# Kernel optimization log

Hardware: AMD Instinct MI355X
Metric: run time of the kernel (lower is better)

Reference implementation:

```python
import jax, jax.numpy as jnp
import numpy as np

N = 65536
E = 1048576
IN_DIM, HID, OUT = 500, 256, 64
ALPHA = 0.1
K = 10


def setup_inputs() -> dict:
    key = jax.random.key(0)
    ks = jax.random.split(key, 12)
    x = jax.random.normal(ks[0], (N, IN_DIM), dtype=jnp.float32)
    edge_row = jax.random.randint(ks[1], (E,), 0, N, dtype=jnp.int32)
    edge_col = jax.random.randint(ks[2], (E,), 0, N, dtype=jnp.int32)
    edge_weight = jax.random.uniform(ks[3], (E,), dtype=jnp.float32)
    # Linear params (Kaiming-uniform-like scale)
    def lin(k, fan_in, fan_out):
        kw, kb = jax.random.split(k)
        bound = 1.0 / np.sqrt(fan_in)
        W = jax.random.uniform(kw, (fan_in, fan_out), minval=-bound, maxval=bound, dtype=jnp.float32)
        b = jax.random.uniform(kb, (fan_out,), minval=-bound, maxval=bound, dtype=jnp.float32)
        return W, b
    W1, b1 = lin(ks[4], IN_DIM, HID)
    W2, b2 = lin(ks[5], HID, HID)
    W3, b3 = lin(ks[6], HID, OUT)
    return {"x": x, "W1": W1, "b1": b1, "W2": W2, "b2": b2,
            "W3": W3, "b3": b3, "edge_weight": edge_weight,
            "edge_row": edge_row, "edge_col": edge_col}


def reference(x, W1, b1, W2, b2, W3, b3, edge_weight, edge_row, edge_col):
    # MLP stack (dropout=0.0, norm_type='none')
    h = jax.nn.relu(x @ W1 + b1)          # [N, HID]
    h = jax.nn.relu(h @ W2 + b2)          # [N, HID]
    h = h @ W3 + b3                        # [N, OUT]
    h0 = h
    w = edge_weight[:, None]               # [E, 1]
    # APPNP: k steps of h = (1-alpha) * (A @ h) + alpha * h0 (SpMM via segment_sum)
    def step(h, _):
        msg = h[edge_col] * w               # [E, OUT] gather + scale
        agg = jax.ops.segment_sum(msg, edge_row, num_segments=N)  # [N, OUT]
        return (1.0 - ALPHA) * agg + ALPHA * h0, None
    h, _ = jax.lax.scan(step, h, None, length=K)
    return h
```

## Files before the change

kernel.cpp:

```cpp
#include <hip/hip_runtime.h>
#include <cstdint>
#include <cstddef>


#define N_NODES   65536
#define N_EDGES   1048576
#define IN_DIM    500
#define IN_PAD    512
#define HID_DIM   256
#define OUT_DIM   64
#define K_STEPS   10

#define NPW   8
#define CAPW  608
#define NCHUNK 16

typedef _Float16 half8 __attribute__((ext_vector_type(8)));
typedef __fp16   fp16x2 __attribute__((ext_vector_type(2)));
typedef float    f32x4 __attribute__((ext_vector_type(4)));

#define HA_OFF    0ULL
#define HB_OFF    33554432ULL
#define H1_OFF    67108864ULL
#define H0_OFF    67108864ULL
#define H2_OFF    100663296ULL
#define CNT2_OFF  100663296ULL
#define RANK_OFF  104857600ULL
#define TOT_OFF   109051904ULL
#define W1T_OFF   134217728ULL
#define W2T_OFF   134479872ULL
#define W3T_OFF   134610944ULL
#define ROWP_OFF  134643712ULL
#define EDG_OFF   135430400ULL

__device__ __forceinline__ void gload_lds16(const void* g, void* l) {
  __builtin_amdgcn_global_load_lds(
      (const __attribute__((address_space(1))) void*)g,
      (__attribute__((address_space(3))) void*)l, 16, 0, 0);
}

__device__ __forceinline__ unsigned short f2bf_rne(float f) {
  unsigned u = __float_as_uint(f);
  u += 0x7fffu + ((u >> 16) & 1u);
  return (unsigned short)(u >> 16);
}
__device__ __forceinline__ float uaf(unsigned u) {
  return __uint_as_float(u);
}
__device__ __forceinline__ float lo16(unsigned v) {
  return __uint_as_float(v << 16);
}
__device__ __forceinline__ float hi16(unsigned v) {
  return __uint_as_float(v & 0xffff0000u);
}

template <int TM, int TN, int WM, int WN, bool RELU, int OMODE>
__global__ __launch_bounds__(256)
void gemm_kernel(const _Float16* __restrict__ A, const _Float16* __restrict__ B,
                 const float* __restrict__ bias, void* __restrict__ Cout,
                 int M, int Nn, int K) {
  static_assert((TM * 8) % 256 == 0 && (TN * 8) % 256 == 0, "tile");
  __shared__ uint4 As[TM * 8];
  __shared__ uint4 Bs[TN * 8];
  const int t    = threadIdx.x;
  const int lane = t & 63;
  const int wave = t >> 6;
  const int wm   = wave / WN;
  const int wn   = wave % WN;
  const int row0 = blockIdx.x * TM;
  const int col0 = blockIdx.y * TN;
  const int l15  = lane & 15;
  const int lq   = lane >> 4;

  f32x4 acc[4][4];
#pragma unroll
  for (int i = 0; i < 4; ++i)
#pragma unroll
    for (int j = 0; j < 4; ++j) acc[i][j] = (f32x4){0.f, 0.f, 0.f, 0.f};

  for (int k0 = 0; k0 < K; k0 += 64) {
#pragma unroll
    for (int i = 0; i < (TM * 8) / 256; ++i) {
      const int c = i * 256 + wave * 64 + lane;
      const int q = c / TM;
      const int r = c % TM;
      gload_lds16(A + (size_t)(row0 + r) * K + (k0 + q * 8),
                  As + i * 256 + wave * 64);
    }
#pragma unroll
    for (int i = 0; i < (TN * 8) / 256; ++i) {
      const int c = i * 256 + wave * 64 + lane;
      const int q = c / TN;
      const int r = c % TN;
      gload_lds16(B + (size_t)(col0 + r) * K + (k0 + q * 8),
                  Bs + i * 256 + wave * 64);
    }
    __syncthreads();
#pragma unroll
    for (int kk = 0; kk < 2; ++kk) {
      const int qa = kk * 4 + lq;
      half8 af[4], bfr[4];
#pragma unroll
      for (int mt = 0; mt < 4; ++mt)
        af[mt] = *((const half8*)(As + (qa * TM + wm * 64 + mt * 16 + l15)));
#pragma unroll
      for (int nt = 0; nt < 4; ++nt)
        bfr[nt] = *((const half8*)(Bs + (qa * TN + wn * 64 + nt * 16 + l15)));
#pragma unroll
      for (int mt = 0; mt < 4; ++mt)
#pragma unroll
        for (int nt = 0; nt < 4; ++nt)
          acc[mt][nt] = __builtin_amdgcn_mfma_f32_16x16x32_f16(
              af[mt], bfr[nt], acc[mt][nt], 0, 0, 0);
    }
    __syncthreads();
  }

#pragma unroll
  for (int mt = 0; mt < 4; ++mt) {
#pragma unroll
    for (int nt = 0; nt < 4; ++nt) {
      const int col = col0 + wn * 64 + nt * 16 + l15;
      const float bv = bias[col];
#pragma unroll
      for (int r = 0; r < 4; ++r) {
        const int row = row0 + wm * 64 + mt * 16 + lq * 4 + r;
        float v = acc[mt][nt][r] + bv;
        if (RELU) v = fmaxf(v, 0.f);
        if (OMODE == 0)
          ((_Float16*)Cout)[(size_t)row * Nn + col] = (_Float16)v;
        else if (OMODE == 1)
          ((unsigned short*)Cout)[(size_t)row * Nn + col] = f2bf_rne(v);
        else
          ((float*)Cout)[(size_t)row * Nn + col] = v;
      }
    }
  }
}

__global__ __launch_bounds__(256)
void gemm1_f32(const float* __restrict__ x, const _Float16* __restrict__ B,
               const float* __restrict__ bias, _Float16* __restrict__ C) {
  __shared__ uint4 As[16 * 128];
  __shared__ uint4 Bs[8 * 256];
  const int t    = threadIdx.x;
  const int lane = t & 63;
  const int wave = t >> 6;
  const int row0 = blockIdx.x * 128;
  const int l15  = lane & 15;
  const int lq   = lane >> 4;

  f32x4 acc[8][4];
#pragma unroll
  for (int i = 0; i < 8; ++i)
#pragma unroll
    for (int j = 0; j < 4; ++j) acc[i][j] = (f32x4){0.f, 0.f, 0.f, 0.f};

  for (int k0 = 0; k0 < IN_PAD; k0 += 64) {
#pragma unroll
    for (int i = 0; i < 8; ++i) {
      const int c = i * 256 + t;
      const int q = c >> 7;
      const int r = c & 127;
      int kb = k0 + q * 4;
      if (kb >= IN_DIM) kb = 0;
      gload_lds16(x + (size_t)(row0 + r) * IN_DIM + kb, As + q * 128 + r);
    }
#pragma unroll
    for (int i = 0; i < 8; ++i) {
      const int c = i * 256 + t;
      const int q = c >> 8;
      const int r = c & 255;
      gload_lds16(B + (size_t)r * IN_PAD + (k0 + q * 8), Bs + q * 256 + r);
    }
    __syncthreads();
#pragma unroll
    for (int kk = 0; kk < 2; ++kk) {
      const int qa = kk * 4 + lq;
      half8 bfr[4];
#pragma unroll
      for (int nt = 0; nt < 4; ++nt)
        bfr[nt] = *((const half8*)(Bs + qa * 256 + wave * 64 + nt * 16 + l15));
#pragma unroll
      for (int mt = 0; mt < 8; ++mt) {
        const uint4 lo = As[(qa * 2 + 0) * 128 + mt * 16 + l15];
        const uint4 hi = As[(qa * 2 + 1) * 128 + mt * 16 + l15];
        half8 af;
        fp16x2 p;
        p = __builtin_amdgcn_cvt_pkrtz(uaf(lo.x), uaf(lo.y));
        af[0] = p[0]; af[1] = p[1];
        p = __builtin_amdgcn_cvt_pkrtz(uaf(lo.z), uaf(lo.w));
        af[2] = p[0]; af[3] = p[1];
        p = __builtin_amdgcn_cvt_pkrtz(uaf(hi.x), uaf(hi.y));
        af[4] = p[0]; af[5] = p[1];
        p = __builtin_amdgcn_cvt_pkrtz(uaf(hi.z), uaf(hi.w));
        af[6] = p[0]; af[7] = p[1];
#pragma unroll
        for (int nt = 0; nt < 4; ++nt)
          acc[mt][nt] = __builtin_amdgcn_mfma_f32_16x16x32_f16(
              af, bfr[nt], acc[mt][nt], 0, 0, 0);
      }
    }
    __syncthreads();
  }

#pragma unroll
  for (int mt = 0; mt < 8; ++mt) {
#pragma unroll
    for (int nt = 0; nt < 4; ++nt) {
      const int col = wave * 64 + nt * 16 + l15;
      const float bv = bias[col];
#pragma unroll
      for (int r = 0; r < 4; ++r) {
        const int row = row0 + mt * 16 + lq * 4 + r;
        const float v = fmaxf(acc[mt][nt][r] + bv, 0.f);
        C[(size_t)row * HID_DIM + col] = (_Float16)v;
      }
    }
  }
}

__global__ void cast_w_kernel(const float* __restrict__ W,
                              _Float16* __restrict__ Wt, int K, int Kpad,
                              int Nn) {
  const int idx = blockIdx.x * blockDim.x + threadIdx.x;
  if (idx >= Nn * Kpad) return;
  const int n = idx / Kpad;
  const int k = idx % Kpad;
  const float v = (k < K) ? W[(size_t)k * Nn + n] : 0.f;
  Wt[idx] = (_Float16)v;
}

__global__ void hist2_kernel(const int* __restrict__ row,
                             int* __restrict__ cnt2, int* __restrict__ rank,
                             int E) {
  const int e = blockIdx.x * blockDim.x + threadIdx.x;
  if (e < E)
    rank[e] = atomicAdd(&cnt2[(e >> 16) * N_NODES + row[e]], 1);
}

__global__ void scan_tot_kernel(const int* __restrict__ cnt2,
                                int* __restrict__ tot) {
  const int r = blockIdx.x * blockDim.x + threadIdx.x;
  int s = 0;
#pragma unroll
  for (int c = 0; c < NCHUNK; ++c) s += cnt2[c * N_NODES + r];
  tot[r] = s;
}

__global__ void scan_kernel(const int4* __restrict__ counts4,
                            int* __restrict__ rowptr) {
  __shared__ int part[1024];
  const int t = threadIdx.x;
  const int base = t * 16;
  int4 c[16];
  int s = 0;
#pragma unroll
  for (int i = 0; i < 16; ++i) {
    c[i] = counts4[base + i];
    s += c[i].x + c[i].y + c[i].z + c[i].w;
  }
  part[t] = s;
  __syncthreads();
  for (int off = 1; off < 1024; off <<= 1) {
    const int v = (t >= off) ? part[t - off] : 0;
    __syncthreads();
    part[t] += v;
    __syncthreads();
  }
  int run = (t == 0) ? 0 : part[t - 1];
#pragma unroll
  for (int i = 0; i < 16; ++i) {
    int4 r;
    r.x = run; run += c[i].x;
    r.y = run; run += c[i].y;
    r.z = run; run += c[i].z;
    r.w = run; run += c[i].w;
    ((int4*)rowptr)[base + i] = r;
  }
  if (t == 1023) rowptr[N_NODES] = run;
}

__global__ void chunkbase_kernel(int* __restrict__ cnt2,
                                 const int* __restrict__ rowptr) {
  const int r = blockIdx.x * blockDim.x + threadIdx.x;
  int run = rowptr[r];
#pragma unroll
  for (int c = 0; c < NCHUNK; ++c) {
    const int t = cnt2[c * N_NODES + r];
    cnt2[c * N_NODES + r] = run;
    run += t;
  }
}

__global__ void scatter2_kernel(const int* __restrict__ row,
                                const int* __restrict__ col,
                                const float* __restrict__ w,
                                const int* __restrict__ rank,
                                const int* __restrict__ cbase,
                                int2* __restrict__ edges, int E) {
  const int e = blockIdx.x * blockDim.x + threadIdx.x;
  if (e < E) {
    const int pos = cbase[(e >> 16) * N_NODES + row[e]] + rank[e];
    edges[pos] = make_int2(col[e], __float_as_int(w[e]));
  }
}

template <bool OUT_F32>
__global__ __launch_bounds__(256)
void prop_step(const unsigned short* __restrict__ hin,
               const unsigned short* __restrict__ h0,
               void* __restrict__ hout, const int* __restrict__ rowptr,
               const int2* __restrict__ edges) {
  __shared__ int2 eb[4][CAPW];
  const int wave = threadIdx.x >> 6;
  const int lane = threadIdx.x & 63;
  const int half = lane >> 5;
  const int lp   = lane & 31;
  const int node0 = (blockIdx.x * 4 + wave) * NPW;
  const unsigned* __restrict__ hin32 = (const unsigned*)hin;
  const unsigned* __restrict__ h032  = (const unsigned*)h0;

  const int rp  = rowptr[node0 + min(lane, NPW)];
  const int beg = __shfl(rp, 0);
  const int nE  = __shfl(rp, NPW) - beg;
  const int rrel = rp - beg;
  int2* __restrict__ ebw = eb[wave];

  const bool fast = (nE <= CAPW);
  if (fast) {
    for (int i = lane; i < nE; i += 64) ebw[i] = edges[beg + i];
    __builtin_amdgcn_s_waitcnt(0);
  }

  for (int i = 0; i < NPW; ++i) {
    const int nb = __shfl(rrel, i);
    const int ne = __shfl(rrel, i + 1);
    float ax0 = 0.f, ay0 = 0.f, ax1 = 0.f, ay1 = 0.f;
    int j = nb;
    if (fast) {
      for (; j + 8 <= ne; j += 8) {
        const int2 e0 = ebw[j + 0 + half];
        const int2 e1 = ebw[j + 2 + half];
        const int2 e2 = ebw[j + 4 + half];
        const int2 e3 = ebw[j + 6 + half];
        const unsigned v0 = hin32[(e0.x << 5) | lp];
        const unsigned v1 = hin32[(e1.x << 5) | lp];
        const unsigned v2 = hin32[(e2.x << 5) | lp];
        const unsigned v3 = hin32[(e3.x << 5) | lp];
        const float w0 = uaf(e0.y), w1 = uaf(e1.y);
        const float w2 = uaf(e2.y), w3 = uaf(e3.y);
        ax0 = fmaf(w0, lo16(v0), ax0); ay0 = fmaf(w0, hi16(v0), ay0);
        ax1 = fmaf(w1, lo16(v1), ax1); ay1 = fmaf(w1, hi16(v1), ay1);
        ax0 = fmaf(w2, lo16(v2), ax0); ay0 = fmaf(w2, hi16(v2), ay0);
        ax1 = fmaf(w3, lo16(v3), ax1); ay1 = fmaf(w3, hi16(v3), ay1);
      }
      for (; j + 2 <= ne; j += 2) {
        const int2 e = ebw[j + half];
        const unsigned v = hin32[(e.x << 5) | lp];
        const float w = uaf(e.y);
        ax0 = fmaf(w, lo16(v), ax0); ay0 = fmaf(w, hi16(v), ay0);
      }
      if (j < ne) {
        const int2 e = ebw[j];
        const unsigned v = hin32[(e.x << 5) | lp];
        const float w = half ? 0.f : uaf(e.y);
        ax0 = fmaf(w, lo16(v), ax0); ay0 = fmaf(w, hi16(v), ay0);
      }
    } else {
      for (; j < ne; j += 2) {
        const int idx = j + half;
        const int2 e = edges[beg + (idx < ne ? idx : ne - 1)];
        const float w = (idx < ne) ? uaf(e.y) : 0.f;
        const unsigned v = hin32[(e.x << 5) | lp];
        ax0 = fmaf(w, lo16(v), ax0); ay0 = fmaf(w, hi16(v), ay0);
      }
    }
    float sx = ax0 + ax1;
    float sy = ay0 + ay1;
    sx += __shfl_xor(sx, 32);
    sy += __shfl_xor(sy, 32);
    const int o32 = ((node0 + i) << 5) | lp;
    const unsigned h0v = h032[o32];
    const float r0 = 0.9f * sx + 0.1f * lo16(h0v);
    const float r1 = 0.9f * sy + 0.1f * hi16(h0v);
    if (half == 0) {
      if (OUT_F32) {
        ((float2*)hout)[o32] = make_float2(r0, r1);
      } else {
        ((unsigned*)hout)[o32] =
            (unsigned)f2bf_rne(r0) | ((unsigned)f2bf_rne(r1) << 16);
      }
    }
  }
}

extern "C" void kernel_launch(void* const* d_in, const int* in_sizes, int n_in,
                              void* d_out, int out_size, void* d_ws,
                              size_t ws_size, hipStream_t stream) {
  const float* x  = (const float*)d_in[0];
  const float* W1 = (const float*)d_in[1];
  const float* b1 = (const float*)d_in[2];
  const float* W2 = (const float*)d_in[3];
  const float* b2 = (const float*)d_in[4];
  const float* W3 = (const float*)d_in[5];
  const float* b3 = (const float*)d_in[6];
  const float* ew = (const float*)d_in[7];
  const int* erow = (const int*)d_in[8];
  const int* ecol = (const int*)d_in[9];

  char* ws = (char*)d_ws;
  _Float16* h1  = (_Float16*)(ws + H1_OFF);
  _Float16* h2  = (_Float16*)(ws + H2_OFF);
  _Float16* w1t = (_Float16*)(ws + W1T_OFF);
  _Float16* w2t = (_Float16*)(ws + W2T_OFF);
  _Float16* w3t = (_Float16*)(ws + W3T_OFF);
  unsigned short* h0b = (unsigned short*)(ws + H0_OFF);
  unsigned short* hAb = (unsigned short*)(ws + HA_OFF);
  unsigned short* hBb = (unsigned short*)(ws + HB_OFF);
  int* rowp     = (int*)(ws + ROWP_OFF);
  int* cnt2     = (int*)(ws + CNT2_OFF);
  int* rankb    = (int*)(ws + RANK_OFF);
  int* tot      = (int*)(ws + TOT_OFF);
  int2* edges   = (int2*)(ws + EDG_OFF);
  float* outp   = (float*)d_out;

  hipMemsetAsync(cnt2, 0, NCHUNK * N_NODES * sizeof(int), stream);
  hist2_kernel<<<N_EDGES / 256, 256, 0, stream>>>(erow, cnt2, rankb, N_EDGES);
  scan_tot_kernel<<<N_NODES / 256, 256, 0, stream>>>(cnt2, tot);
  scan_kernel<<<1, 1024, 0, stream>>>((const int4*)tot, rowp);
  chunkbase_kernel<<<N_NODES / 256, 256, 0, stream>>>(cnt2, rowp);
  scatter2_kernel<<<N_EDGES / 256, 256, 0, stream>>>(erow, ecol, ew, rankb,
                                                     cnt2, edges, N_EDGES);

  cast_w_kernel<<<(HID_DIM * IN_PAD) / 256, 256, 0, stream>>>(W1, w1t, IN_DIM,
                                                              IN_PAD, HID_DIM);
  cast_w_kernel<<<(HID_DIM * HID_DIM) / 256, 256, 0, stream>>>(
      W2, w2t, HID_DIM, HID_DIM, HID_DIM);
  cast_w_kernel<<<(OUT_DIM * HID_DIM) / 256, 256, 0, stream>>>(
      W3, w3t, HID_DIM, HID_DIM, OUT_DIM);

  gemm1_f32<<<dim3(N_NODES / 128), 256, 0, stream>>>(x, w1t, b1, h1);
  gemm_kernel<128, 128, 2, 2, true, 0>
      <<<dim3(N_NODES / 128, HID_DIM / 128), 256, 0, stream>>>(
          h1, w2t, b2, h2, N_NODES, HID_DIM, HID_DIM);
  gemm_kernel<256, 64, 4, 1, false, 1>
      <<<dim3(N_NODES / 256, 1), 256, 0, stream>>>(h2, w3t, b3, h0b, N_NODES,
                                                   OUT_DIM, HID_DIM);

  for (int s = 0; s < K_STEPS - 1; ++s) {
    const unsigned short* hin = (s == 0) ? h0b : ((s - 1) & 1 ? hBb : hAb);
    unsigned short* hout = (s & 1) ? hBb : hAb;
    prop_step<false><<<N_NODES / (4 * NPW), 256, 0, stream>>>(hin, h0b, hout,
                                                              rowp, edges);
  }
  prop_step<true><<<N_NODES / (4 * NPW), 256, 0, stream>>>(
      (K_STEPS - 2) & 1 ? hBb : hAb, h0b, outp, rowp, edges);
}
```

Measured before the change: 629.2 us.

## Fuse all propagation steps into one cooperative persistent kernel with grid sync

Replaces the ten separate prop_step launches with one cooperative kernel. It loops over the K steps and calls grid.sync between them, ping-ponging the bf16 buffers and writing fp32 output on the last step. Each wave now handles 16 nodes with a larger LDS edge buffer, so its edge slice is loaded into LDS once and reused across all steps instead of being reread from global memory each step. In exchange it pays grid-wide barrier costs and caps residency at 4 blocks per CU. The launch only works if all 1024 blocks can be co-resident, and fewer waves are left to hide gather latency.

Result: slower. 1.822 ms (+189.5%).

```diff
diff --git a/kernel.cpp b/kernel.cpp
--- a/kernel.cpp
+++ b/kernel.cpp
@@ -1,6 +1,9 @@
 #include <hip/hip_runtime.h>
+#include <hip/hip_cooperative_groups.h>
 #include <cstdint>
 #include <cstddef>
+
+namespace cg = cooperative_groups;
 
 
 #define N_NODES   65536
@@ -11,8 +14,8 @@
 #define OUT_DIM   64
 #define K_STEPS   10
 
-#define NPW   8
-#define CAPW  608
+#define NPW   16
+#define CAPW  1152
 #define NCHUNK 16
 
 typedef _Float16 half8 __attribute__((ext_vector_type(8)));
@@ -306,20 +309,18 @@
   }
 }
 
-template <bool OUT_F32>
-__global__ __launch_bounds__(256)
-void prop_step(const unsigned short* __restrict__ hin,
-               const unsigned short* __restrict__ h0,
-               void* __restrict__ hout, const int* __restrict__ rowptr,
+__global__ __launch_bounds__(256, 4)
+void prop_coop(const unsigned* __restrict__ h0g,
+               unsigned* __restrict__ hA, unsigned* __restrict__ hB,
+               float* __restrict__ outp, const int* __restrict__ rowptr,
                const int2* __restrict__ edges) {
   __shared__ int2 eb[4][CAPW];
+  cg::grid_group grid = cg::this_grid();
   const int wave = threadIdx.x >> 6;
   const int lane = threadIdx.x & 63;
   const int half = lane >> 5;
   const int lp   = lane & 31;
   const int node0 = (blockIdx.x * 4 + wave) * NPW;
-  const unsigned* __restrict__ hin32 = (const unsigned*)hin;
-  const unsigned* __restrict__ h032  = (const unsigned*)h0;
 
   const int rp  = rowptr[node0 + min(lane, NPW)];
   const int beg = __shfl(rp, 0);
@@ -333,65 +334,73 @@
     __builtin_amdgcn_s_waitcnt(0);
   }
 
-  for (int i = 0; i < NPW; ++i) {
-    const int nb = __shfl(rrel, i);
-    const int ne = __shfl(rrel, i + 1);
-    float ax0 = 0.f, ay0 = 0.f, ax1 = 0.f, ay1 = 0.f;
-    int j = nb;
-    if (fast) {
-      for (; j + 8 <= ne; j += 8) {
-        const int2 e0 = ebw[j + 0 + half];
-        const int2 e1 = ebw[j + 2 + half];
-        const int2 e2 = ebw[j + 4 + half];
-        const int2 e3 = ebw[j + 6 + half];
-        const unsigned v0 = hin32[(e0.x << 5) | lp];
-        const unsigned v1 = hin32[(e1.x << 5) | lp];
-        const unsigned v2 = hin32[(e2.x << 5) | lp];
-        const unsigned v3 = hin32[(e3.x << 5) | lp];
-        const float w0 = uaf(e0.y), w1 = uaf(e1.y);
-        const float w2 = uaf(e2.y), w3 = uaf(e3.y);
-        ax0 = fmaf(w0, lo16(v0), ax0); ay0 = fmaf(w0, hi16(v0), ay0);
-        ax1 = fmaf(w1, lo16(v1), ax1); ay1 = fmaf(w1, hi16(v1), ay1);
-        ax0 = fmaf(w2, lo16(v2), ax0); ay0 = fmaf(w2, hi16(v2), ay0);
-        ax1 = fmaf(w3, lo16(v3), ax1); ay1 = fmaf(w3, hi16(v3), ay1);
+  for (int s = 0; s < K_STEPS; ++s) {
+    const bool last = (s == K_STEPS - 1);
+    const unsigned* __restrict__ hin32 =
+        (s == 0) ? h0g : (((s - 1) & 1) ? hB : hA);
+    unsigned* __restrict__ houtb = (s & 1) ? hB : hA;
+
+    for (int i = 0; i < NPW; ++i) {
+      const int nb = __shfl(rrel, i);
+      const int ne = __shfl(rrel, i + 1);
+      float ax0 = 0.f, ay0 = 0.f, ax1 = 0.f, ay1 = 0.f;
+      int j = nb;
+      if (fast) {
+        for (; j + 8 <= ne; j += 8) {
+          const int2 e0 = ebw[j + 0 + half];
+          const int2 e1 = ebw[j + 2 + half];
+          const int2 e2 = ebw[j + 4 + half];
+          const int2 e3 = ebw[j + 6 + half];
+          const unsigned v0 = hin32[(e0.x << 5) | lp];
+          const unsigned v1 = hin32[(e1.x << 5) | lp];
+          const unsigned v2 = hin32[(e2.x << 5) | lp];
+          const unsigned v3 = hin32[(e3.x << 5) | lp];
+          const float w0 = uaf(e0.y), w1 = uaf(e1.y);
+          const float w2 = uaf(e2.y), w3 = uaf(e3.y);
+          ax0 = fmaf(w0, lo16(v0), ax0); ay0 = fmaf(w0, hi16(v0), ay0);
+          ax1 = fmaf(w1, lo16(v1), ax1); ay1 = fmaf(w1, hi16(v1), ay1);
+          ax0 = fmaf(w2, lo16(v2), ax0); ay0 = fmaf(w2, hi16(v2), ay0);
+          ax1 = fmaf(w3, lo16(v3), ax1); ay1 = fmaf(w3, hi16(v3), ay1);
+        }
+        for (; j + 2 <= ne; j += 2) {
+          const int2 e = ebw[j + half];
+          const unsigned v = hin32[(e.x << 5) | lp];
+          const float w = uaf(e.y);
+          ax0 = fmaf(w, lo16(v), ax0); ay0 = fmaf(w, hi16(v), ay0);
+        }
+        if (j < ne) {
+          const int2 e = ebw[j];
+          const unsigned v = hin32[(e.x << 5) | lp];
+          const float w = half ? 0.f : uaf(e.y);
+          ax0 = fmaf(w, lo16(v), ax0); ay0 = fmaf(w, hi16(v), ay0);
+        }
+      } else {
+        for (; j < ne; j += 2) {
+          const int idx = j + half;
+          const int2 e = edges[beg + (idx < ne ? idx : ne - 1)];
+          const float w = (idx < ne) ? uaf(e.y) : 0.f;
+          const unsigned v = hin32[(e.x << 5) | lp];
+          ax0 = fmaf(w, lo16(v), ax0); ay0 = fmaf(w, hi16(v), ay0);
+        }
       }
-      for (; j + 2 <= ne; j += 2) {
-        const int2 e = ebw[j + half];
-        const unsigned v = hin32[(e.x << 5) | lp];
-        const float w = uaf(e.y);
-        ax0 = fmaf(w, lo16(v), ax0); ay0 = fmaf(w, hi16(v), ay0);
+      float sx = ax0 + ax1;
+      float sy = ay0 + ay1;
+      sx += __shfl_xor(sx, 32);
+      sy += __shfl_xor(sy, 32);
+      const int o32 = ((node0 + i) << 5) | lp;
+      const unsigned h0v = h0g[o32];
+      const float r0 = 0.9f * sx + 0.1f * lo16(h0v);
+      const float r1 = 0.9f * sy + 0.1f * hi16(h0v);
+      if (half == 0) {
+        if (last) {
+          ((float2*)outp)[o32] = make_float2(r0, r1);
+        } else {
+          houtb[o32] =
+              (unsigned)f2bf_rne(r0) | ((unsigned)f2bf_rne(r1) << 16);
+        }
       }
-      if (j < ne) {
-        const int2 e = ebw[j];
-        const unsigned v = hin32[(e.x << 5) | lp];
-        const float w = half ? 0.f : uaf(e.y);
-        ax0 = fmaf(w, lo16(v), ax0); ay0 = fmaf(w, hi16(v), ay0);
-      }
-    } else {
-      for (; j < ne; j += 2) {
-        const int idx = j + half;
-        const int2 e = edges[beg + (idx < ne ? idx : ne - 1)];
-        const float w = (idx < ne) ? uaf(e.y) : 0.f;
-        const unsigned v = hin32[(e.x << 5) | lp];
-        ax0 = fmaf(w, lo16(v), ax0); ay0 = fmaf(w, hi16(v), ay0);
-      }
-    }
-    float sx = ax0 + ax1;
-    float sy = ay0 + ay1;
-    sx += __shfl_xor(sx, 32);
-    sy += __shfl_xor(sy, 32);
-    const int o32 = ((node0 + i) << 5) | lp;
-    const unsigned h0v = h032[o32];
-    const float r0 = 0.9f * sx + 0.1f * lo16(h0v);
-    const float r1 = 0.9f * sy + 0.1f * hi16(h0v);
-    if (half == 0) {
-      if (OUT_F32) {
-        ((float2*)hout)[o32] = make_float2(r0, r1);
-      } else {
-        ((unsigned*)hout)[o32] =
-            (unsigned)f2bf_rne(r0) | ((unsigned)f2bf_rne(r1) << 16);
-      }
-    }
+    }
+    if (!last) grid.sync();
   }
 }
 
@@ -416,8 +425,6 @@
   _Float16* w2t = (_Float16*)(ws + W2T_OFF);
   _Float16* w3t = (_Float16*)(ws + W3T_OFF);
   unsigned short* h0b = (unsigned short*)(ws + H0_OFF);
-  unsigned short* hAb = (unsigned short*)(ws + HA_OFF);
-  unsigned short* hBb = (unsigned short*)(ws + HB_OFF);
   int* rowp     = (int*)(ws + ROWP_OFF);
   int* cnt2     = (int*)(ws + CNT2_OFF);
   int* rankb    = (int*)(ws + RANK_OFF);
@@ -448,12 +455,16 @@
       <<<dim3(N_NODES / 256, 1), 256, 0, stream>>>(h2, w3t, b3, h0b, N_NODES,
                                                    OUT_DIM, HID_DIM);
 
-  for (int s = 0; s < K_STEPS - 1; ++s) {
-    const unsigned short* hin = (s == 0) ? h0b : ((s - 1) & 1 ? hBb : hAb);
-    unsigned short* hout = (s & 1) ? hBb : hAb;
-    prop_step<false><<<N_NODES / (4 * NPW), 256, 0, stream>>>(hin, h0b, hout,
-                                                              rowp, edges);
-  }
-  prop_step<true><<<N_NODES / (4 * NPW), 256, 0, stream>>>(
-      (K_STEPS - 2) & 1 ? hBb : hAb, h0b, outp, rowp, edges);
-}
+  {
+    const unsigned* h0u = (const unsigned*)(ws + H0_OFF);
+    unsigned* hAu = (unsigned*)(ws + HA_OFF);
+    unsigned* hBu = (unsigned*)(ws + HB_OFF);
+    const int* rowp_c = rowp;
+    const int2* edges_c = edges;
+    void* kargs[] = {(void*)&h0u, (void*)&hAu, (void*)&hBu,
+                     (void*)&outp, (void*)&rowp_c, (void*)&edges_c};
+    hipLaunchCooperativeKernel((const void*)prop_coop,
+                               dim3(N_NODES / (4 * NPW)), dim3(256), kargs, 0,
+                               stream);
+  }
+}
```

## Load x directly from global in first GEMM, halve row tile

Applied to the files above, without the earlier changes.

The first GEMM no longer stages the fp32 input tile in LDS. Each lane reads its float4 fragments of x straight from global memory and converts them to fp16 for the MFMA, and the row tile shrinks from 128 to 64 so twice as many blocks launch. This removes the LDS staging traffic and lowers LDS and register pressure, aiming for higher occupancy. The cost is that all four waves re-read the same x rows from global memory and the direct reads are less coalesced, so more traffic goes through the L1/L2 caches.

Measured after the change: 687.2 us. 1.09x slower.

```diff
diff --git a/kernel.cpp b/kernel.cpp
--- a/kernel.cpp
+++ b/kernel.cpp
@@ -139,33 +139,23 @@
 }
 
 __global__ __launch_bounds__(256)
-void gemm1_f32(const float* __restrict__ x, const _Float16* __restrict__ B,
-               const float* __restrict__ bias, _Float16* __restrict__ C) {
-  __shared__ uint4 As[16 * 128];
+void gemm1_direct(const float* __restrict__ x, const _Float16* __restrict__ B,
+                  const float* __restrict__ bias, _Float16* __restrict__ C) {
   __shared__ uint4 Bs[8 * 256];
   const int t    = threadIdx.x;
   const int lane = t & 63;
   const int wave = t >> 6;
-  const int row0 = blockIdx.x * 128;
+  const int row0 = blockIdx.x * 64;
   const int l15  = lane & 15;
   const int lq   = lane >> 4;
 
-  f32x4 acc[8][4];
-#pragma unroll
-  for (int i = 0; i < 8; ++i)
+  f32x4 acc[4][4];
+#pragma unroll
+  for (int i = 0; i < 4; ++i)
 #pragma unroll
     for (int j = 0; j < 4; ++j) acc[i][j] = (f32x4){0.f, 0.f, 0.f, 0.f};
 
   for (int k0 = 0; k0 < IN_PAD; k0 += 64) {
-#pragma unroll
-    for (int i = 0; i < 8; ++i) {
-      const int c = i * 256 + t;
-      const int q = c >> 7;
-      const int r = c & 127;
-      int kb = k0 + q * 4;
-      if (kb >= IN_DIM) kb = 0;
-      gload_lds16(x + (size_t)(row0 + r) * IN_DIM + kb, As + q * 128 + r);
-    }
 #pragma unroll
     for (int i = 0; i < 8; ++i) {
       const int c = i * 256 + t;
@@ -177,23 +167,27 @@
 #pragma unroll
     for (int kk = 0; kk < 2; ++kk) {
       const int qa = kk * 4 + lq;
+      const int kb = k0 + qa * 8;
+      const int o1 = (kb     <= IN_DIM - 4) ? kb     : 0;
+      const int o2 = (kb + 4 <= IN_DIM - 4) ? kb + 4 : 0;
       half8 bfr[4];
 #pragma unroll
       for (int nt = 0; nt < 4; ++nt)
         bfr[nt] = *((const half8*)(Bs + qa * 256 + wave * 64 + nt * 16 + l15));
 #pragma unroll
-      for (int mt = 0; mt < 8; ++mt) {
-        const uint4 lo = As[(qa * 2 + 0) * 128 + mt * 16 + l15];
-        const uint4 hi = As[(qa * 2 + 1) * 128 + mt * 16 + l15];
+      for (int mt = 0; mt < 4; ++mt) {
+        const float* src = x + (size_t)(row0 + mt * 16 + l15) * IN_DIM;
+        const float4 a = *(const float4*)(src + o1);
+        const float4 b = *(const float4*)(src + o2);
         half8 af;
         fp16x2 p;
-        p = __builtin_amdgcn_cvt_pkrtz(uaf(lo.x), uaf(lo.y));
+        p = __builtin_amdgcn_cvt_pkrtz(a.x, a.y);
         af[0] = p[0]; af[1] = p[1];
-        p = __builtin_amdgcn_cvt_pkrtz(uaf(lo.z), uaf(lo.w));
+        p = __builtin_amdgcn_cvt_pkrtz(a.z, a.w);
         af[2] = p[0]; af[3] = p[1];
-        p = __builtin_amdgcn_cvt_pkrtz(uaf(hi.x), uaf(hi.y));
+        p = __builtin_amdgcn_cvt_pkrtz(b.x, b.y);
         af[4] = p[0]; af[5] = p[1];
-        p = __builtin_amdgcn_cvt_pkrtz(uaf(hi.z), uaf(hi.w));
+        p = __builtin_amdgcn_cvt_pkrtz(b.z, b.w);
         af[6] = p[0]; af[7] = p[1];
 #pragma unroll
         for (int nt = 0; nt < 4; ++nt)
@@ -205,7 +199,7 @@
   }
 
 #pragma unroll
-  for (int mt = 0; mt < 8; ++mt) {
+  for (int mt = 0; mt < 4; ++mt) {
 #pragma unroll
     for (int nt = 0; nt < 4; ++nt) {
       const int col = wave * 64 + nt * 16 + l15;
@@ -440,7 +434,7 @@
   cast_w_kernel<<<(OUT_DIM * HID_DIM) / 256, 256, 0, stream>>>(
       W3, w3t, HID_DIM, HID_DIM, OUT_DIM);
 
-  gemm1_f32<<<dim3(N_NODES / 128), 256, 0, stream>>>(x, w1t, b1, h1);
+  gemm1_direct<<<dim3(N_NODES / 64), 256, 0, stream>>>(x, w1t, b1, h1);
   gemm_kernel<128, 128, 2, 2, true, 0>
       <<<dim3(N_NODES / 128, HID_DIM / 128), 256, 0, stream>>>(
           h1, w2t, b2, h2, N_NODES, HID_DIM, HID_DIM);
```
